# Performance work log

Measured on AMD Instinct MI355X. Metric: run time of the kernel, lower is better.

The kernel has to match this reference:

```python
import jax, jax.numpy as jnp
import numpy as np
from jax import lax

DN = ('NCHW', 'OIHW', 'NCHW')  # torch conv layout
QMIN, QMAX = -128.0, 127.0     # qint8 range


def setup_inputs() -> dict:
    key = jax.random.key(0)
    k1, k2, k3, k4 = jax.random.split(key, 4)
    B, Cin, Cout, H, W, K = 8, 320, 320, 64, 64, 3
    x = jax.random.normal(k1, (B, Cin, H, W), dtype=jnp.float32)
    # int8 weight values stored as int32 (int_repr of per-channel quantized weight)
    weight_int = jax.random.randint(k2, (Cout, Cin, K, K), -128, 128, dtype=jnp.int32)
    weight_scales = jax.random.uniform(k3, (Cout,), jnp.float32, 0.001, 0.01)
    act_scales = jnp.float32(0.04)        # per-tensor activation scale
    act_zero_points = jnp.float32(3.0)    # per-tensor activation zero point
    act_scales_inv = 1.0 / act_scales
    bias = jax.random.normal(k4, (Cout,), dtype=jnp.float32) * 0.1
    # precomputed buffers (from_float): padding>0 path
    weight_sum_by_input_channels = weight_int.astype(jnp.float32).sum(axis=1, keepdims=True)  # [O,1,K,K]
    scale = weight_scales * act_scales  # fused dequant scale per output channel
    return {
        'x': x,
        'weight_int': weight_int,
        'weight_sum_by_input_channels': weight_sum_by_input_channels,
        'scale': scale,
        'act_scales_inv': act_scales_inv,
        'act_zero_points': act_zero_points,
        'bias': bias,
    }


def reference(x, weight_int, weight_sum_by_input_channels, scale,
              act_scales_inv, act_zero_points, bias):
    stride, pad = 1, 1
    # per-tensor activation quantization: x_int = clamp(round(x/s) + zp)
    x_int = jnp.clip(jnp.round(x * act_scales_inv) + act_zero_points, QMIN, QMAX)
    w = weight_int.astype(jnp.float32)
    # integer conv (emulated in f32): conv(x_int, W_int)
    acc = lax.conv_general_dilated(x_int, w, (stride, stride),
                                   [(pad, pad), (pad, pad)], dimension_numbers=DN)
    # zero-point correction: zp * conv(ones, sum_i W_int) (spatially varying near padding)
    ones = jnp.ones_like(x[:, :1])  # [B,1,H,W]
    corr = lax.conv_general_dilated(ones, weight_sum_by_input_channels, (stride, stride),
                                    [(pad, pad), (pad, pad)], dimension_numbers=DN)
    corr = corr * act_zero_points
    # dequant: per-output-channel scale = w_scale * a_scale, plus float bias
    out = scale[None, :, None, None] * (acc - corr) + bias[None, :, None, None]
    return out
```

## Files before the change

kernel.cpp:

```cpp
#include <hip/hip_runtime.h>
#include <hip/hip_bf16.h>


typedef int v4i __attribute__((ext_vector_type(4)));

typedef const unsigned int __attribute__((address_space(1)))* gas_uptr;
typedef unsigned int __attribute__((address_space(3)))* las_uptr;

#define B_   8
#define CIN  320
#define COUT 320
#define H_   64
#define W_   64
#define HW_  4096
#define HP   66
#define WP   66
#define XPAD_BYTES (B_*HP*WP*CIN)
#define W8_BYTES (COUT*9*CIN)

__global__ __launch_bounds__(256) void repack_bias_kernel(const int* __restrict__ wint,
                                                          unsigned char* __restrict__ w8,
                                                          const float* __restrict__ wsum,
                                                          const float* __restrict__ scale,
                                                          const float* __restrict__ bias,
                                                          const float* __restrict__ zp_p,
                                                          float* __restrict__ be) {
    int j = blockIdx.x * 256 + threadIdx.x;
    if (j < COUT) {
        float s = 0.f;
        #pragma unroll
        for (int tp = 0; tp < 9; ++tp) s += wsum[j*9 + tp];
        be[j] = bias[j] - scale[j] * zp_p[0] * s;
    }
    int co  = j / 720;
    int r   = j - co * 720;
    int tap = r / 80;
    int d   = r - tap * 80;
    int ci  = d * 4;
    const int* base = wint + (co * CIN + ci) * 9 + tap;
    unsigned b0 = (unsigned)(base[0]  & 0xFF);
    unsigned b1 = (unsigned)(base[9]  & 0xFF);
    unsigned b2 = (unsigned)(base[18] & 0xFF);
    unsigned b3 = (unsigned)(base[27] & 0xFF);
    ((unsigned*)w8)[j] = b0 | (b1 << 8) | (b2 << 16) | (b3 << 24);
}

__global__ __launch_bounds__(256) void quant_pad_kernel(const float* __restrict__ x,
                                                        unsigned char* __restrict__ xpad,
                                                        const float* __restrict__ inv_p,
                                                        const float* __restrict__ zp_p) {
    __shared__ __align__(16) unsigned lds[64 * 81];
    int bid = blockIdx.x;
    int b  = bid / HP;
    int ph = bid - b * HP;
    int t  = threadIdx.x;
    float inv = inv_p[0];
    float zp  = zp_p[0];
    int zpi = (int)rintf(zp);
    unsigned zd = ((unsigned)(zpi & 0xFF)) * 0x01010101u;

    unsigned* rowbase = (unsigned*)(xpad + (size_t)((b * HP + ph) * WP) * CIN);

    if (ph == 0 || ph == HP - 1) {
        for (int j = t; j < WP * CIN / 4; j += 256) rowbase[j] = zd;
        return;
    }
    int h = ph - 1;
    const float* xrow = x + (size_t)b * CIN * H_ * W_ + h * W_;
    int wq = t & 15;
    int cg = t >> 4;
    #pragma unroll
    for (int i = 0; i < 5; ++i) {
        int ci0 = i * 64 + cg * 4;
        float4 f[4];
        #pragma unroll
        for (int jj = 0; jj < 4; ++jj)
            f[jj] = *(const float4*)(xrow + (size_t)(ci0 + jj) * HW_ + wq * 4);
        #pragma unroll
        for (int k = 0; k < 4; ++k) {
            unsigned d = 0;
            #pragma unroll
            for (int jj = 0; jj < 4; ++jj) {
                float v = (&f[jj].x)[k];
                float q = rintf(v * inv) + zp;
                q = fminf(fmaxf(q, -128.0f), 127.0f);
                int qi = (int)q;
                d |= ((unsigned)(qi & 0xFF)) << (8 * jj);
            }
            lds[(wq * 4 + k) * 81 + (ci0 >> 2)] = d;
        }
    }
    __syncthreads();
    if (t < 80)            rowbase[t] = zd;
    else if (t < 160)      rowbase[65 * 80 + (t - 80)] = zd;
    for (int j = t; j < 64 * 80; j += 256) {
        int p = j / 80;
        int d = j - p * 80;
        rowbase[80 + j] = lds[p * 81 + d];
    }
}

__global__ __launch_bounds__(256, 2) void conv_gemm_kernel(const unsigned char* __restrict__ xpad,
                                                           const unsigned char* __restrict__ w8,
                                                           const float* __restrict__ scale,
                                                           const float* __restrict__ be,
                                                           float* __restrict__ out) {
    __shared__ __align__(16) unsigned char Al[5 * 128 * 64];

    int t    = threadIdx.x;
    int lane = t & 63;
    int wave = t >> 6;
    int wm   = wave & 1;
    int wn   = wave >> 1;
    int m0   = blockIdx.x * 128;
    int n0   = blockIdx.y * 160;

    int p  = t >> 2;
    int qs = (t & 3) ^ ((p >> 1) & 3);
    int pix0 = m0 + p;
    int pix1 = pix0 + 64;
    int b0i = pix0 >> 12, hw0 = pix0 & 4095;
    int b1i = pix1 >> 12, hw1 = pix1 & 4095;
    const unsigned char* ap0 = xpad + (size_t)(((b0i * HP + (hw0 >> 6)) * WP + (hw0 & 63)) * CIN) + qs * 16;
    const unsigned char* ap1 = xpad + (size_t)(((b1i * HP + (hw1 >> 6)) * WP + (hw1 & 63)) * CIN) + qs * 16;

    int colc = lane & 15;
    int q    = lane >> 4;
    int aAddr[4];
    #pragma unroll
    for (int mi = 0; mi < 4; ++mi) {
        int P = wm * 64 + mi * 16 + colc;
        aAddr[mi] = P * 64 + ((q ^ ((P >> 1) & 3)) * 16);
    }

    const unsigned char* bptr[5];
    #pragma unroll
    for (int ni = 0; ni < 5; ++ni) {
        int co = n0 + wn * 80 + ni * 16 + colc;
        bptr[ni] = w8 + (size_t)co * (9 * CIN) + q * 16;
    }

    v4i acc[4][5];
    v4i zero = {0, 0, 0, 0};
    #pragma unroll
    for (int mi = 0; mi < 4; ++mi)
        #pragma unroll
        for (int ni = 0; ni < 5; ++ni) acc[mi][ni] = zero;

    #pragma unroll 1
    for (int kh = 0; kh < 3; ++kh) {
        #pragma unroll 1
        for (int kw = 0; kw < 3; ++kw) {
            int aoff = (kh * WP + kw) * CIN;
            int boff = (kh * 3 + kw) * CIN;

            v4i bf[5][5];
            #pragma unroll
            for (int c5 = 0; c5 < 5; ++c5)
                #pragma unroll
                for (int ni = 0; ni < 5; ++ni)
                    bf[c5][ni] = *(const v4i*)(bptr[ni] + boff + c5 * 64);

            #pragma unroll
            for (int c5 = 0; c5 < 5; ++c5) {
                __builtin_amdgcn_global_load_lds((gas_uptr)(const void*)(ap0 + aoff + c5 * 64),
                                                 (las_uptr)(Al + c5 * 8192 + t * 16), 16, 0, 0);
                __builtin_amdgcn_global_load_lds((gas_uptr)(const void*)(ap1 + aoff + c5 * 64),
                                                 (las_uptr)(Al + c5 * 8192 + 4096 + t * 16), 16, 0, 0);
            }
            __syncthreads();

            #pragma unroll
            for (int c5 = 0; c5 < 5; ++c5) {
                v4i a[4];
                #pragma unroll
                for (int mi = 0; mi < 4; ++mi)
                    a[mi] = *(const v4i*)(Al + c5 * 8192 + aAddr[mi]);
                #pragma unroll
                for (int mi = 0; mi < 4; ++mi)
                    #pragma unroll
                    for (int ni = 0; ni < 5; ++ni)
                        acc[mi][ni] = __builtin_amdgcn_mfma_i32_16x16x64_i8(a[mi], bf[c5][ni], acc[mi][ni], 0, 0, 0);
            }
            __syncthreads();
        }
    }

    #pragma unroll
    for (int ni = 0; ni < 5; ++ni) {
        int co = n0 + wn * 80 + ni * 16 + colc;
        float s  = scale[co];
        float bz = be[co];
        #pragma unroll
        for (int mi = 0; mi < 4; ++mi) {
            int pix = m0 + wm * 64 + mi * 16 + q * 4;
            int bb2 = pix >> 12;
            int hw  = pix & 4095;
            v4i v = acc[mi][ni];
            float4 o;
            o.x = s * (float)v.x + bz;
            o.y = s * (float)v.y + bz;
            o.z = s * (float)v.z + bz;
            o.w = s * (float)v.w + bz;
            *(float4*)(out + (size_t)(bb2 * COUT + co) * HW_ + hw) = o;
        }
    }
}

extern "C" void kernel_launch(void* const* d_in, const int* in_sizes, int n_in,
                              void* d_out, int out_size, void* d_ws, size_t ws_size,
                              hipStream_t stream) {
    const float* x     = (const float*)d_in[0];
    const int*   wint  = (const int*)d_in[1];
    const float* wsum  = (const float*)d_in[2];
    const float* scale = (const float*)d_in[3];
    const float* inv_p = (const float*)d_in[4];
    const float* zp_p  = (const float*)d_in[5];
    const float* bias  = (const float*)d_in[6];
    float* out = (float*)d_out;

    unsigned char* xpad = (unsigned char*)d_ws;
    unsigned char* w8   = xpad + XPAD_BYTES;
    float*         be   = (float*)(w8 + W8_BYTES);

    repack_bias_kernel<<<(COUT * 720) / 256, 256, 0, stream>>>(wint, w8, wsum, scale, bias, zp_p, be);
    quant_pad_kernel<<<B_ * HP, 256, 0, stream>>>(x, xpad, inv_p, zp_p);

    dim3 grid((B_ * H_ * W_) / 128, COUT / 160);
    conv_gemm_kernel<<<grid, 256, 0, stream>>>(xpad, w8, scale, be, out);
}
```

Before: 159.3 us.

## Stage padded input halo once per channel chunk and reuse across all nine taps

Instead of reloading a 128-pixel A tile from global memory for each of the nine filter taps, the conv GEMM loads a 4-row by 66-column halo of padded input per 64-channel chunk into LDS. All nine kernel taps are computed from that halo by shifted LDS reads. The channel-chunk loop is double-buffered so the next chunk's global-to-LDS load overlaps the current MFMAs, and barriers drop from two per tap to one per chunk. The cost is more LDS use and extra slot-index arithmetic. Weight fragments are now loaded per tap inside the unrolled loop, with less register prefetch.

```diff
diff --git a/kernel.cpp b/kernel.cpp
--- a/kernel.cpp
+++ b/kernel.cpp
@@ -100,12 +100,16 @@
     }
 }
 
+#define CHUNK_SLOTS 1056
+#define ROUNDS 5
+#define BUF_BYTES (ROUNDS * 256 * 16)
+
 __global__ __launch_bounds__(256, 2) void conv_gemm_kernel(const unsigned char* __restrict__ xpad,
                                                            const unsigned char* __restrict__ w8,
                                                            const float* __restrict__ scale,
                                                            const float* __restrict__ be,
                                                            float* __restrict__ out) {
-    __shared__ __align__(16) unsigned char Al[5 * 128 * 64];
+    __shared__ __align__(16) unsigned char Al[2 * BUF_BYTES];
 
     int t    = threadIdx.x;
     int lane = t & 63;
@@ -114,24 +118,24 @@
     int wn   = wave >> 1;
     int m0   = blockIdx.x * 128;
     int n0   = blockIdx.y * 160;
-
-    int p  = t >> 2;
-    int qs = (t & 3) ^ ((p >> 1) & 3);
-    int pix0 = m0 + p;
-    int pix1 = pix0 + 64;
-    int b0i = pix0 >> 12, hw0 = pix0 & 4095;
-    int b1i = pix1 >> 12, hw1 = pix1 & 4095;
-    const unsigned char* ap0 = xpad + (size_t)(((b0i * HP + (hw0 >> 6)) * WP + (hw0 & 63)) * CIN) + qs * 16;
-    const unsigned char* ap1 = xpad + (size_t)(((b1i * HP + (hw1 >> 6)) * WP + (hw1 & 63)) * CIN) + qs * 16;
+    int b0   = m0 >> 12;
+    int h0   = (m0 & 4095) >> 6;
+
+    int srcoff[ROUNDS];
+    #pragma unroll
+    for (int r = 0; r < ROUNDS; ++r) {
+        int slot = r * 256 + t;
+        if (slot >= CHUNK_SLOTS) slot = 0;
+        int R   = slot / 264;
+        int rem = slot - R * 264;
+        int C   = rem >> 2;
+        int ql  = rem & 3;
+        int qs  = ql ^ (C & 3);
+        srcoff[r] = ((b0 * HP + h0 + R) * WP + C) * CIN + qs * 16;
+    }
 
     int colc = lane & 15;
     int q    = lane >> 4;
-    int aAddr[4];
-    #pragma unroll
-    for (int mi = 0; mi < 4; ++mi) {
-        int P = wm * 64 + mi * 16 + colc;
-        aAddr[mi] = P * 64 + ((q ^ ((P >> 1) & 3)) * 16);
-    }
 
     const unsigned char* bptr[5];
     #pragma unroll
@@ -147,43 +151,48 @@
         #pragma unroll
         for (int ni = 0; ni < 5; ++ni) acc[mi][ni] = zero;
 
+    #pragma unroll
+    for (int r = 0; r < ROUNDS; ++r)
+        __builtin_amdgcn_global_load_lds((gas_uptr)(const void*)(xpad + srcoff[r]),
+                                         (las_uptr)(Al + r * 4096 + t * 16), 16, 0, 0);
+    __syncthreads();
+
     #pragma unroll 1
-    for (int kh = 0; kh < 3; ++kh) {
-        #pragma unroll 1
-        for (int kw = 0; kw < 3; ++kw) {
-            int aoff = (kh * WP + kw) * CIN;
-            int boff = (kh * 3 + kw) * CIN;
-
-            v4i bf[5][5];
+    for (int c = 0; c < 5; ++c) {
+        if (c < 4) {
+            unsigned char* dst = Al + ((c + 1) & 1) * BUF_BYTES;
+            int ci = (c + 1) * 64;
             #pragma unroll
-            for (int c5 = 0; c5 < 5; ++c5)
+            for (int r = 0; r < ROUNDS; ++r)
+                __builtin_amdgcn_global_load_lds((gas_uptr)(const void*)(xpad + srcoff[r] + ci),
+                                                 (las_uptr)(dst + r * 4096 + t * 16), 16, 0, 0);
+        }
+        const unsigned char* ab = Al + (c & 1) * BUF_BYTES;
+        int coff = c * 64;
+
+        #pragma unroll
+        for (int kh = 0; kh < 3; ++kh) {
+            #pragma unroll
+            for (int kw = 0; kw < 3; ++kw) {
+                v4i bf[5];
                 #pragma unroll
                 for (int ni = 0; ni < 5; ++ni)
-                    bf[c5][ni] = *(const v4i*)(bptr[ni] + boff + c5 * 64);
-
-            #pragma unroll
-            for (int c5 = 0; c5 < 5; ++c5) {
-                __builtin_amdgcn_global_load_lds((gas_uptr)(const void*)(ap0 + aoff + c5 * 64),
-                                                 (las_uptr)(Al + c5 * 8192 + t * 16), 16, 0, 0);
-                __builtin_amdgcn_global_load_lds((gas_uptr)(const void*)(ap1 + aoff + c5 * 64),
-                                                 (las_uptr)(Al + c5 * 8192 + 4096 + t * 16), 16, 0, 0);
-            }
-            __syncthreads();
-
-            #pragma unroll
-            for (int c5 = 0; c5 < 5; ++c5) {
+                    bf[ni] = *(const v4i*)(bptr[ni] + (kh * 3 + kw) * CIN + coff);
                 v4i a[4];
                 #pragma unroll
-                for (int mi = 0; mi < 4; ++mi)
-                    a[mi] = *(const v4i*)(Al + c5 * 8192 + aAddr[mi]);
+                for (int mi = 0; mi < 4; ++mi) {
+                    int C = mi * 16 + colc + kw;
+                    a[mi] = *(const v4i*)(ab + (wm + kh) * 4224 + C * 64
+                                             + ((q ^ (C & 3)) * 16));
+                }
                 #pragma unroll
                 for (int mi = 0; mi < 4; ++mi)
                     #pragma unroll
                     for (int ni = 0; ni < 5; ++ni)
-                        acc[mi][ni] = __builtin_amdgcn_mfma_i32_16x16x64_i8(a[mi], bf[c5][ni], acc[mi][ni], 0, 0, 0);
+                        acc[mi][ni] = __builtin_amdgcn_mfma_i32_16x16x64_i8(a[mi], bf[ni], acc[mi][ni], 0, 0, 0);
             }
-            __syncthreads();
-        }
+        }
+        __syncthreads();
     }
 
     #pragma unroll
```

Measured after the change: 148.0 us. 7.1% less time.
